# Performance work log

Hardware: AMD Instinct MI355X
Metric: run time of the kernel (lower is better)

Reference implementation:

```python
import jax, jax.numpy as jnp
import numpy as np

EPS = 1e-12
IMU_NOISE_DIAG = np.array([1e-07, 1e-07, 0.01, 0.001], dtype=np.float32)
INIT_COVAR_SQRT = np.array([0, 0, 0, 0, 0, 0, 0.01, 0.01, 0.01, 1e-4, 1e-4, 1e-4,
                            1e-08, 1e-08, 1e-08, 0.1, 0.1, 0.1], dtype=np.float32)
TRANS_SCALE = 5.4
TS2 = TRANS_SCALE * TRANS_SCALE
VIS_INIT_GUESS = 10.0 / TS2
VIS_BETA, VIS_GAMMA = 3.0, 1.0
IMU_BETA, IMU_GAMMA = 4.0, 1.0


def skew3(v):  # (..., 3) -> (..., 3, 3)
    x, y, z = v[..., 0], v[..., 1], v[..., 2]
    o = jnp.zeros_like(x)
    return jnp.stack([jnp.stack([o, -z, y], -1),
                      jnp.stack([z, o, -x], -1),
                      jnp.stack([-y, x, o], -1)], -2)


def exp_SO3(phi):  # (..., 3) -> (..., 3, 3) Rodrigues
    theta2 = jnp.sum(phi * phi, axis=-1)
    theta = jnp.sqrt(theta2)
    small = theta < 1e-8
    th = jnp.where(small, 1.0, theta)
    A = jnp.where(small, 1.0 - theta2 / 6.0, jnp.sin(th) / th)[..., None, None]
    B = jnp.where(small, 0.5 - theta2 / 24.0, (1.0 - jnp.cos(th)) / (th * th))[..., None, None]
    K = skew3(phi)
    return jnp.eye(3, dtype=phi.dtype) + A * K + B * (K @ K)


def force_symmetrical(M):
    Mu = jnp.triu(M)
    n = M.shape[-1]
    return Mu + jnp.swapaxes(Mu, -1, -2) * (1.0 - jnp.eye(n, dtype=M.dtype))


def proc_vis_covar(vis_std):
    # vis_covar_scale is all ones (par.vis_covar_scale = 1.0)
    scale = jnp.ones((6,), dtype=vis_std.dtype)
    diag = VIS_INIT_GUESS * (10.0 ** (VIS_BETA * jnp.tanh(VIS_GAMMA * vis_std)))
    diag = diag / scale[None, :]
    return jax.vmap(jnp.diag)(diag)  # (2B, 6, 6)


def get_imu_noise_covar(imu_noise_weight):
    # Linear(1,4,bias=False) applied to ones(1): just the weight column
    covar = 10.0 ** (IMU_BETA * jnp.tanh(IMU_GAMMA * imu_noise_weight[:, 0]))  # (4,)
    diag = jnp.repeat(jnp.asarray(IMU_NOISE_DIAG), 3) * jnp.repeat(covar, 3)   # (12,)
    return jnp.diag(diag)


def propagate(dts, wa_xyzs, R_ckbts, g_k, imu_noise_covar, P0):
    B = dts.shape[0]
    T = dts.shape[1]
    I3 = jnp.eye(3, dtype=dts.dtype)
    I18 = jnp.eye(18, dtype=dts.dtype)

    def step(P, inp):
        dt, gyro, accel, R = inp  # (B,), (B,3), (B,3), (B,3,3)
        Rt = jnp.swapaxes(R, -1, -2)
        w = gyro  # bw_k = 0
        Rg = jnp.einsum('bij,bj->bi', Rt, g_k)
        a = accel - Rg  # ba_k = 0
        F = jnp.zeros((B, 18, 18), dtype=dt.dtype)
        F = F.at[:, 0:3, 0:3].set(-skew3(w))
        F = F.at[:, 0:3, 12:15].set(-I3)
        F = F.at[:, 3:6, 6:9].set(I3)
        F = F.at[:, 6:9, 0:3].set(-jnp.einsum('bij,bjk->bik', R, skew3(Rg + a)))
        F = F.at[:, 6:9, 9:12].set(-I3)
        F = F.at[:, 6:9, 15:18].set(-R)
        G = jnp.zeros((B, 18, 12), dtype=dt.dtype)
        G = G.at[:, 0:3, 0:3].set(-I3)
        G = G.at[:, 6:9, 6:9].set(-R)
        G = G.at[:, 12:15, 3:6].set(I3)
        G = G.at[:, 15:18, 9:12].set(I3)
        dtb = dt[:, None, None]
        Phi = I18 + F * dtb + 0.5 * (F @ F) * (dtb * dtb)
        Phi = Phi.at[:, 0:3, 0:3].set(jnp.swapaxes(exp_SO3(dt[:, None] * w), -1, -2))
        PhiT = jnp.swapaxes(Phi, -1, -2)
        Q = (Phi @ G @ imu_noise_covar @ jnp.swapaxes(G, -1, -2) @ PhiT) * dtb
        P = force_symmetrical(Phi @ P @ PhiT + Q)
        return P, None

    xs = (jnp.swapaxes(dts, 0, 1),                       # (T, B)
          jnp.swapaxes(wa_xyzs[:, :T, :3], 0, 1),        # (T, B, 3)
          jnp.swapaxes(wa_xyzs[:, :T, 3:], 0, 1),        # (T, B, 3)
          jnp.swapaxes(R_ckbts[:, :T], 0, 1))            # (T, B, 3, 3)
    P, _ = jax.lax.scan(step, P0, xs)
    return P


def update(preimu_rot, preimu_trans, P, vis_rot, vis_trans, vis_covar, H0, H1, v_ck, g_ck):
    B = vis_rot.shape[0]
    residual = jnp.concatenate([vis_rot - preimu_rot, vis_trans - preimu_trans], axis=1)  # (B,6)
    I3 = jnp.eye(3, dtype=vis_rot.dtype)
    H = jnp.zeros((B, 6, 18), dtype=vis_rot.dtype)
    H = H.at[:, 0:3, 0:3].set(H0)
    H = H.at[:, 3:6, 0:3].set(H1)
    H = H.at[:, 3:6, 3:6].set(I3)
    Ht = jnp.swapaxes(H, -1, -2)
    S = H @ P @ Ht + vis_covar                 # (B,6,6)
    K = P @ Ht @ jnp.linalg.inv(S)             # (B,18,6)
    est = K @ residual[..., None]              # (B,18,1)
    phi_e, p_e = est[:, 0:3], est[:, 3:6]
    v_e, g_e = est[:, 6:9], est[:, 9:12]
    ekf_phi = preimu_rot + (H0 @ phi_e)[..., 0]
    ekf_t = preimu_trans + (H1 @ phi_e)[..., 0] + p_e[..., 0]
    return ekf_phi, ekf_t, v_ck + v_e[..., 0], g_ck + g_e[..., 0]


def setup_inputs() -> dict:
    key = jax.random.key(0)
    ks = jax.random.split(key, 16)
    B2 = 8192
    d = {
        'dts': jax.random.uniform(ks[0], (B2, 11), jnp.float32) * 0.01,
        'wa_xyzs': jax.random.normal(ks[1], (B2, 12, 6), jnp.float32),
        'R_ckbts': jax.random.normal(ks[2], (B2, 12, 3, 3), jnp.float32),
        'velocities': jax.random.normal(ks[3], (B2, 3), jnp.float32),
        'gravities': jax.random.normal(ks[4], (B2, 3), jnp.float32),
        'H0': jax.random.normal(ks[5], (B2, 3, 3), jnp.float32),
        'H1': jax.random.normal(ks[6], (B2, 3, 3), jnp.float32),
        'preimu_rot': jax.random.normal(ks[7], (B2, 3), jnp.float32),
        'preimu_trans': jax.random.normal(ks[8], (B2, 3), jnp.float32),
        'vis_rot': jax.random.normal(ks[9], (B2, 3), jnp.float32),
        'vis_trans': jax.random.normal(ks[10], (B2, 3), jnp.float32),
        'vis_rot_std': jax.random.uniform(ks[11], (B2, 3), jnp.float32),
        'vis_trans_std': jax.random.uniform(ks[12], (B2, 3), jnp.float32),
        'init_covar_diag_sqrt': jnp.asarray(INIT_COVAR_SQRT),
        'imu_noise_weight': jnp.zeros((4, 1), jnp.float32),  # train_imu_noise_covar=False -> zeroed
    }
    return d


def reference(dts, wa_xyzs, R_ckbts, velocities, gravities, H0, H1,
              preimu_rot, preimu_trans, vis_rot, vis_trans,
              vis_rot_std, vis_trans_std, init_covar_diag_sqrt, imu_noise_weight):
    B2 = dts.shape[0]
    vis_std = jnp.concatenate([vis_rot_std, vis_trans_std], axis=1)
    vis_covar = proc_vis_covar(vis_std)
    vis_trans = vis_trans * TRANS_SCALE
    imu_noise_covar = get_imu_noise_covar(imu_noise_weight)
    P0_diag = init_covar_diag_sqrt * init_covar_diag_sqrt + EPS
    P0 = jnp.broadcast_to(jnp.diag(P0_diag), (B2, 18, 18))
    P = propagate(dts, wa_xyzs, R_ckbts, gravities, imu_noise_covar, P0)
    ekf_phi, ekf_t, ekf_v, ekf_g = update(preimu_rot, preimu_trans, P,
                                          vis_rot, vis_trans, vis_covar,
                                          H0, H1, velocities, gravities)
    return jnp.concatenate([ekf_phi, ekf_t, ekf_v, ekf_g], axis=1)  # (2B, 12)
```

## Files before the change

### kernel.cpp

```cpp
#include <hip/hip_runtime.h>
#include <math.h>

#define TSTEPS 11
#define PPB 7
#define LPP 9
#define IN_STRIDE 228
#define WSTRIDE 228
#define PHT_OFF 0
#define S6_OFF 144
#define Y_OFF 192
#define EST_OFF 200

#define FENCE_RAW() asm volatile("s_waitcnt lgkmcnt(0)" ::: "memory")
#define FENCE_WAR() asm volatile("" ::: "memory")

__device__ __forceinline__ float sel3(int c, float a, float b, float d) {
    float t = (c == 1) ? b : a;
    return (c == 2) ? d : t;
}

__device__ __forceinline__ size_t umin_sz(size_t a, size_t b) { return a < b ? a : b; }

__global__ void __launch_bounds__(64)
ekf_kernel(const float* __restrict__ dts, const float* __restrict__ wa,
           const float* __restrict__ Rc, const float* __restrict__ vel,
           const float* __restrict__ grav, const float* __restrict__ H0g,
           const float* __restrict__ H1g, const float* __restrict__ prot,
           const float* __restrict__ ptrans, const float* __restrict__ vrot,
           const float* __restrict__ vtrans, const float* __restrict__ vrstd,
           const float* __restrict__ vtstd, const float* __restrict__ icds,
           const float* __restrict__ inw, float* __restrict__ out, int B)
{
    __shared__ __align__(16) float gin[PPB * IN_STRIDE];
    __shared__ __align__(16) float lds[PPB * WSTRIDE];
    const int tid = threadIdx.x;
    const int praw = tid / LPP;
    const int r = tid - praw * LPP;
    const int p = (praw < PPB) ? praw : (PPB - 1);
    const int blk0 = blockIdx.x * PPB;
    const int b0 = blk0 + p;
    const bool valid = (praw < PPB) && (b0 < B);
    const int b = (b0 < B) ? b0 : (B - 1);
    float* L = lds + p * WSTRIDE;
    const float* gi = gin + p * IN_STRIDE;

    {
        const size_t dmax = (size_t)B * 11 - 1;
        for (int e = tid; e < PPB * 11; e += 64) {
            const int pp = e / 11, o = e - pp * 11;
            gin[pp * IN_STRIDE + o * 20] = dts[umin_sz((size_t)blk0 * 11 + e, dmax)];
        }
        const size_t wmax = (size_t)B * 72 - 1;
        for (int e = tid; e < PPB * 66; e += 64) {
            const int pp = e / 66, o = e - pp * 66;
            const int t = o / 6, k = o - t * 6;
            gin[pp * IN_STRIDE + t * 20 + 2 + k] =
                wa[umin_sz((size_t)blk0 * 72 + (size_t)pp * 72 + o, wmax)];
        }
        const size_t rmax = (size_t)B * 108 - 1;
        for (int e = tid; e < PPB * 99; e += 64) {
            const int pp = e / 99, o = e - pp * 99;
            const int t = o / 9, k = o - t * 9;
            gin[pp * IN_STRIDE + t * 20 + 8 + k] =
                Rc[umin_sz((size_t)blk0 * 108 + (size_t)pp * 108 + o, rmax)];
        }
    }

    float h0v[9], h1v[9];
#pragma unroll
    for (int i = 0; i < 9; ++i) { h0v[i] = H0g[(size_t)b * 9 + i]; h1v[i] = H1g[(size_t)b * 9 + i]; }
    const int rc6 = (r < 6) ? r : 5;
    const float* hpr = (rc6 < 3) ? (H0g + (size_t)b * 9 + rc6 * 3)
                                 : (H1g + (size_t)b * 9 + (rc6 - 3) * 3);
    const float hr0 = hpr[0], hr1 = hpr[1], hr2 = hpr[2];
    const float sdv = (rc6 < 3) ? vrstd[(size_t)b * 3 + rc6] : vtstd[(size_t)b * 3 + (rc6 - 3)];
    const float rsa = (rc6 < 3) ? vrot[(size_t)b * 3 + rc6] : vtrans[(size_t)b * 3 + (rc6 - 3)];
    const float rsb = (rc6 < 3) ? prot[(size_t)b * 3 + rc6] : ptrans[(size_t)b * 3 + (rc6 - 3)];
    const float velv = vel[(size_t)b * 3 + ((r >= 6) ? (r - 6) : 0)];

    const float qcA = 1e-7f * exp10f(4.f * tanhf(inw[0]));
    const float qcB = 1e-7f * exp10f(4.f * tanhf(inw[1]));
    const float qcC = 1e-2f * exp10f(4.f * tanhf(inw[2]));
    const float qcD = 1e-3f * exp10f(4.f * tanhf(inw[3]));

    const float g0 = grav[(size_t)b*3+0], g1 = grav[(size_t)b*3+1], g2 = grav[(size_t)b*3+2];

    float np[18], ncr[9];
#pragma unroll
    for (int k = 0; k < 18; ++k) np[k] = 0.f;
#pragma unroll
    for (int k = 0; k < 9; ++k) ncr[k] = 0.f;
    float d_br;
    { const float d0 = icds[r];     np[r] = d0*d0 + 1e-12f;
      const float d1 = icds[9 + r]; d_br  = d1*d1 + 1e-12f; }

    const int cls = (r < 3) ? 0 : ((r < 6) ? 1 : 2);
    const int c3 = r - 3 * cls;

    FENCE_RAW();

    float dt = gi[0];
    float w0, w1, w2, ar0, ar1, ar2, Rm[9];
    {
        const float2 qa = *(const float2*)&gi[2];
        const float2 qb = *(const float2*)&gi[4];
        const float2 qc = *(const float2*)&gi[6];
        w0 = qa.x; w1 = qa.y; w2 = qb.x; ar0 = qb.y; ar1 = qc.x; ar2 = qc.y;
        const float4 r0 = *(const float4*)&gi[8];
        const float4 r1 = *(const float4*)&gi[12];
        Rm[0]=r0.x; Rm[1]=r0.y; Rm[2]=r0.z; Rm[3]=r0.w;
        Rm[4]=r1.x; Rm[5]=r1.y; Rm[6]=r1.z; Rm[7]=r1.w;
        Rm[8]=gi[16];
    }

    for (int t = 0; t < TSTEPS; ++t) {
        const int tn = (t + 1 < TSTEPS) ? (t + 1) : t;
        const float dt_n = gi[tn*20];
        const float2 nqa = *(const float2*)&gi[tn*20 + 2];
        const float2 nqb = *(const float2*)&gi[tn*20 + 4];
        const float2 nqc = *(const float2*)&gi[tn*20 + 6];
        const float4 nr0 = *(const float4*)&gi[tn*20 + 8];
        const float4 nr1 = *(const float4*)&gi[tn*20 + 12];
        const float nr8 = gi[tn*20 + 16];

        const float hdt2 = 0.5f * dt * dt;
        const float Rg0 = Rm[0]*g0 + Rm[3]*g1 + Rm[6]*g2;
        const float Rg1 = Rm[1]*g0 + Rm[4]*g1 + Rm[7]*g2;
        const float Rg2 = Rm[2]*g0 + Rm[5]*g1 + Rm[8]*g2;
        const float a0 = Rg0 + (ar0 - Rg0);
        const float a1 = Rg1 + (ar1 - Rg1);
        const float a2 = Rg2 + (ar2 - Rg2);

        const float p0 = dt*w0, p1 = dt*w1, p2 = dt*w2;
        const float th2 = p0*p0 + p1*p1 + p2*p2;
        const float th4 = th2 * th2;
        const float A  = 1.f - th2*(1.f/6.f)  + th4*(1.f/120.f);
        const float Bc = 0.5f - th2*(1.f/24.f) + th4*(1.f/720.f);
        float E[9];
        E[0] =  Bc*(p0*p0 - th2);  E[1] =  A*p2 + Bc*p0*p1;  E[2] = -A*p1 + Bc*p0*p2;
        E[3] = -A*p2 + Bc*p1*p0;   E[4] =  Bc*(p1*p1 - th2); E[5] =  A*p0 + Bc*p1*p2;
        E[6] =  A*p1 + Bc*p2*p0;   E[7] = -A*p0 + Bc*p2*p1;  E[8] =  Bc*(p2*p2 - th2);
        float N[9];
        N[0] = -(Rm[1]*a2 - Rm[2]*a1);  N[1] = -(Rm[2]*a0 - Rm[0]*a2);  N[2] = -(Rm[0]*a1 - Rm[1]*a0);
        N[3] = -(Rm[4]*a2 - Rm[5]*a1);  N[4] = -(Rm[5]*a0 - Rm[3]*a2);  N[5] = -(Rm[3]*a1 - Rm[4]*a0);
        N[6] = -(Rm[7]*a2 - Rm[8]*a1);  N[7] = -(Rm[8]*a0 - Rm[6]*a2);  N[8] = -(Rm[6]*a1 - Rm[7]*a0);
        float M2[9];
#pragma unroll
        for (int c = 0; c < 3; ++c) {
            const float n0 = N[c*3], n1 = N[c*3+1], n2 = N[c*3+2];
            M2[c*3+0] = dt*n0 - hdt2*(n1*w2 - n2*w1);
            M2[c*3+1] = dt*n1 - hdt2*(n2*w0 - n0*w2);
            M2[c*3+2] = dt*n2 - hdt2*(n0*w1 - n1*w0);
        }

        auto Smv = [&](const float v[18], float o[9]) {
            const float ev0 = E[0]*v[0] + E[1]*v[1] + E[2]*v[2];
            const float ev1 = E[3]*v[0] + E[4]*v[1] + E[5]*v[2];
            const float ev2 = E[6]*v[0] + E[7]*v[1] + E[8]*v[2];
            const float cx0 = w1*v[14] - w2*v[13];
            const float cx1 = w2*v[12] - w0*v[14];
            const float cx2 = w0*v[13] - w1*v[12];
            o[0] = ev0 - dt*v[12] + hdt2*cx0;
            o[1] = ev1 - dt*v[13] + hdt2*cx1;
            o[2] = ev2 - dt*v[14] + hdt2*cx2;
            const float nv0 = N[0]*v[0] + N[1]*v[1] + N[2]*v[2];
            const float nv1 = N[3]*v[0] + N[4]*v[1] + N[5]*v[2];
            const float nv2 = N[6]*v[0] + N[7]*v[1] + N[8]*v[2];
            const float rv0 = Rm[0]*v[15] + Rm[1]*v[16] + Rm[2]*v[17];
            const float rv1 = Rm[3]*v[15] + Rm[4]*v[16] + Rm[5]*v[17];
            const float rv2 = Rm[6]*v[15] + Rm[7]*v[16] + Rm[8]*v[17];
            o[3] = hdt2*nv0 + dt*v[6] - hdt2*v[9]  - hdt2*rv0;
            o[4] = hdt2*nv1 + dt*v[7] - hdt2*v[10] - hdt2*rv1;
            o[5] = hdt2*nv2 + dt*v[8] - hdt2*v[11] - hdt2*rv2;
            const float mv0 = M2[0]*v[0] + M2[1]*v[1] + M2[2]*v[2];
            const float mv1 = M2[3]*v[0] + M2[4]*v[1] + M2[5]*v[2];
            const float mv2 = M2[6]*v[0] + M2[7]*v[1] + M2[8]*v[2];
            const float nw0 = N[0]*v[12] + N[1]*v[13] + N[2]*v[14];
            const float nw1 = N[3]*v[12] + N[4]*v[13] + N[5]*v[14];
            const float nw2 = N[6]*v[12] + N[7]*v[13] + N[8]*v[14];
            o[6] = mv0 - dt*v[9]  - hdt2*nw0 - dt*rv0;
            o[7] = mv1 - dt*v[10] - hdt2*nw1 - dt*rv1;
            o[8] = mv2 - dt*v[11] - hdt2*nw2 - dt*rv2;
        };

        float uca[9];
        Smv(np, uca);

        float ucb[9];
        {
            const float colR0 = sel3(c3, Rm[0], Rm[1], Rm[2]);
            const float colR1 = sel3(c3, Rm[3], Rm[4], Rm[5]);
            const float colR2 = sel3(c3, Rm[6], Rm[7], Rm[8]);
            const float colN0 = sel3(c3, N[0], N[1], N[2]);
            const float colN1 = sel3(c3, N[3], N[4], N[5]);
            const float colN2 = sel3(c3, N[6], N[7], N[8]);
            const float colK0 = sel3(c3, 0.f, -w2,  w1);
            const float colK1 = sel3(c3,  w2, 0.f, -w0);
            const float colK2 = sel3(c3, -w1,  w0, 0.f);
            const float e0c = (c3 == 0) ? 1.f : 0.f;
            const float e1c = (c3 == 1) ? 1.f : 0.f;
            const float e2c = (c3 == 2) ? 1.f : 0.f;
            const float dbdt = d_br * dt, dbh = d_br * hdt2;

            const float s00 = (cls == 1) ? (-dbdt*e0c + dbh*colK0) : 0.f;
            const float s01 = (cls == 1) ? (-dbdt*e1c + dbh*colK1) : 0.f;
            const float s02 = (cls == 1) ? (-dbdt*e2c + dbh*colK2) : 0.f;
            const float s30 = (cls == 0) ? -dbh*e0c : ((cls == 2) ? -dbh*colR0 : 0.f);
            const float s31 = (cls == 0) ? -dbh*e1c : ((cls == 2) ? -dbh*colR1 : 0.f);
            const float s32 = (cls == 0) ? -dbh*e2c : ((cls == 2) ? -dbh*colR2 : 0.f);
            const float s60 = (cls == 0) ? -dbdt*e0c : ((cls == 1) ? -dbh*colN0 : -dbdt*colR0);
            const float s61 = (cls == 0) ? -dbdt*e1c : ((cls == 1) ? -dbh*colN1 : -dbdt*colR1);
            const float s62 = (cls == 0) ? -dbdt*e2c : ((cls == 1) ? -dbh*colN2 : -dbdt*colR2);

            ucb[0] = E[0]*ncr[0] + E[1]*ncr[1] + E[2]*ncr[2] + s00;
            ucb[1] = E[3]*ncr[0] + E[4]*ncr[1] + E[5]*ncr[2] + s01;
            ucb[2] = E[6]*ncr[0] + E[7]*ncr[1] + E[8]*ncr[2] + s02;
            ucb[3] = hdt2*(N[0]*ncr[0] + N[1]*ncr[1] + N[2]*ncr[2]) + dt*ncr[6] + s30;
            ucb[4] = hdt2*(N[3]*ncr[0] + N[4]*ncr[1] + N[5]*ncr[2]) + dt*ncr[7] + s31;
            ucb[5] = hdt2*(N[6]*ncr[0] + N[7]*ncr[1] + N[8]*ncr[2]) + dt*ncr[8] + s32;
            ucb[6] = M2[0]*ncr[0] + M2[1]*ncr[1] + M2[2]*ncr[2] + s60;
            ucb[7] = M2[3]*ncr[0] + M2[4]*ncr[1] + M2[5]*ncr[2] + s61;
            ucb[8] = M2[6]*ncr[0] + M2[7]*ncr[1] + M2[8]*ncr[2] + s62;
        }

#pragma unroll
        for (int i = 0; i < 9; ++i) {
            L[i*20 + r]     = uca[i];
            L[i*20 + 9 + r] = ucb[i];
        }
        FENCE_RAW();

        float ur[18];
        {
            const float4* up = (const float4*)&L[r*20];
            const float4 q0 = up[0], q1 = up[1], q2 = up[2], q3 = up[3];
            const float2 q4 = *(const float2*)&L[r*20 + 16];
            ur[0]=q0.x; ur[1]=q0.y; ur[2]=q0.z; ur[3]=q0.w;
            ur[4]=q1.x; ur[5]=q1.y; ur[6]=q1.z; ur[7]=q1.w;
            ur[8]=q2.x; ur[9]=q2.y; ur[10]=q2.z; ur[11]=q2.w;
            ur[12]=q3.x; ur[13]=q3.y; ur[14]=q3.z; ur[15]=q3.w;
            ur[16]=q4.x; ur[17]=q4.y;
        }

        const float rc0 = sel3(c3, Rm[0], Rm[3], Rm[6]);
        const float rc1 = sel3(c3, Rm[1], Rm[4], Rm[7]);
        const float rc2 = sel3(c3, Rm[2], Rm[5], Rm[8]);
        const float dq = dt * qcC;
        const float q0v = dq * (Rm[0]*rc0 + Rm[1]*rc1 + Rm[2]*rc2);
        const float q1v = dq * (Rm[3]*rc0 + Rm[4]*rc1 + Rm[5]*rc2);
        const float q2v = dq * (Rm[6]*rc0 + Rm[7]*rc1 + Rm[8]*rc2);

        float w9[9];
        Smv(ur, w9);

#pragma unroll
        for (int i = 0; i < 9; ++i)
            np[i] = np[i] + uca[i] + ur[i] + w9[i];
        if (r < 3) np[r] += dt * qcA;
        if (r >= 6) { np[6] += q0v; np[7] += q1v; np[8] += q2v; }
#pragma unroll
        for (int i = 9; i < 18; ++i) np[i] += ur[i];

#pragma unroll
        for (int i = 0; i < 9; ++i) ncr[i] += ucb[i];
        if (r >= 3) d_br += dt * ((r < 6) ? qcB : qcD);

        FENCE_WAR();

        dt = dt_n;
        w0 = nqa.x; w1 = nqa.y; w2 = nqb.x; ar0 = nqb.y; ar1 = nqc.x; ar2 = nqc.y;
        Rm[0]=nr0.x; Rm[1]=nr0.y; Rm[2]=nr0.z; Rm[3]=nr0.w;
        Rm[4]=nr1.x; Rm[5]=nr1.y; Rm[6]=nr1.z; Rm[7]=nr1.w;
        Rm[8]=nr8;
    }

    float phtA[6], phtB[6];
#pragma unroll
    for (int m = 0; m < 3; ++m) {
        phtA[m] = np[0]*h0v[m*3] + np[1]*h0v[m*3+1] + np[2]*h0v[m*3+2];
        phtB[m] = ncr[0]*h0v[m*3] + ncr[1]*h0v[m*3+1] + ncr[2]*h0v[m*3+2];
    }
#pragma unroll
    for (int m = 3; m < 6; ++m) {
        phtA[m] = np[0]*h1v[(m-3)*3] + np[1]*h1v[(m-3)*3+1] + np[2]*h1v[(m-3)*3+2] + np[m];
        phtB[m] = ncr[0]*h1v[(m-3)*3] + ncr[1]*h1v[(m-3)*3+1] + ncr[2]*h1v[(m-3)*3+2] + ncr[m];
    }
#pragma unroll
    for (int m = 0; m < 6; ++m) {
        L[PHT_OFF + r*8 + m]       = phtA[m];
        L[PHT_OFF + (9 + r)*8 + m] = phtB[m];
    }
    FENCE_RAW();

    if (valid && r < 6) {
        const float VIG = (float)(10.0 / (5.4 * 5.4));
#pragma unroll
        for (int n = 0; n < 6; ++n) {
            float v = hr0 * L[PHT_OFF + 0*8 + n] + hr1 * L[PHT_OFF + 1*8 + n]
                    + hr2 * L[PHT_OFF + 2*8 + n];
            if (r >= 3) v += phtA[n];
            if (n == r) v += VIG * exp10f(3.f * tanhf(sdv));
            L[S6_OFF + r*8 + n] = v;
        }
        L[S6_OFF + r*8 + 6] = (r < 3) ? (rsa - rsb) : (rsa * 5.4f - rsb);
    }
    FENCE_RAW();

    if (valid && r == 0) {
        float a[6][7];
        const float* Sb = &L[S6_OFF];
#pragma unroll
        for (int m = 0; m < 6; ++m) {
            const float4 q0 = *(const float4*)&Sb[m*8];
            const float4 q1 = *(const float4*)&Sb[m*8 + 4];
            a[m][0]=q0.x; a[m][1]=q0.y; a[m][2]=q0.z; a[m][3]=q0.w;
            a[m][4]=q1.x; a[m][5]=q1.y; a[m][6]=q1.z;
        }
#pragma unroll
        for (int k = 0; k < 6; ++k) {
#pragma unroll
            for (int j = k + 1; j < 6; ++j) {
                const bool c = fabsf(a[j][k]) > fabsf(a[k][k]);
#pragma unroll
                for (int cc = k; cc < 7; ++cc) {
                    const float hi = c ? a[j][cc] : a[k][cc];
                    const float lo = c ? a[k][cc] : a[j][cc];
                    a[k][cc] = hi; a[j][cc] = lo;
                }
            }
            const float inv = 1.f / a[k][k];
#pragma unroll
            for (int j = 0; j < 6; ++j) {
                if (j == k) continue;
                const float f = a[j][k] * inv;
#pragma unroll
                for (int cc = k + 1; cc < 7; ++cc) a[j][cc] -= f * a[k][cc];
            }
        }
#pragma unroll
        for (int m = 0; m < 6; ++m) L[Y_OFF + m] = a[m][6] / a[m][m];
    }
    FENCE_RAW();

    float ym[6];
#pragma unroll
    for (int m = 0; m < 6; ++m) ym[m] = L[Y_OFF + m];
    float estr = 0.f, est9 = 0.f;
#pragma unroll
    for (int m = 0; m < 6; ++m) { estr += phtA[m]*ym[m]; est9 += phtB[m]*ym[m]; }
    if (valid) {
        L[EST_OFF + r] = estr;
        if (r < 3) L[EST_OFF + 9 + r] = est9;
    }
    FENCE_RAW();

    const float e0 = L[EST_OFF + 0], e1 = L[EST_OFF + 1], e2 = L[EST_OFF + 2];
    if (valid) {
        float o;
        if (r < 3) {
            o = rsb + hr0*e0 + hr1*e1 + hr2*e2;
        } else if (r < 6) {
            o = rsb + hr0*e0 + hr1*e1 + hr2*e2 + estr;
        } else {
            o = velv + estr;
        }
        out[(size_t)b*12 + r] = o;
        if (r < 3) out[(size_t)b*12 + 9 + r] = ((r==0)?g0:((r==1)?g1:g2)) + est9;
    }
}

extern "C" void kernel_launch(void* const* d_in, const int* in_sizes, int n_in,
                              void* d_out, int out_size, void* d_ws, size_t ws_size,
                              hipStream_t stream) {
    const float* dts    = (const float*)d_in[0];
    const float* wa     = (const float*)d_in[1];
    const float* Rc     = (const float*)d_in[2];
    const float* vel    = (const float*)d_in[3];
    const float* grav   = (const float*)d_in[4];
    const float* H0g    = (const float*)d_in[5];
    const float* H1g    = (const float*)d_in[6];
    const float* prot   = (const float*)d_in[7];
    const float* ptrans = (const float*)d_in[8];
    const float* vrot   = (const float*)d_in[9];
    const float* vtrans = (const float*)d_in[10];
    const float* vrstd  = (const float*)d_in[11];
    const float* vtstd  = (const float*)d_in[12];
    const float* icds   = (const float*)d_in[13];
    const float* inw    = (const float*)d_in[14];
    float* outp = (float*)d_out;

    const int B = in_sizes[0] / TSTEPS;
    const int grid = (B + PPB - 1) / PPB;
    hipLaunchKernelGGL(ekf_kernel, dim3(grid), dim3(64), 0, stream,
                       dts, wa, Rc, vel, grav, H0g, H1g, prot, ptrans,
                       vrot, vtrans, vrstd, vtstd, icds, inw, outp, B);
}
```

Measured before the change: 34.50 us.

## Process two EKF problems per lane group to interleave independent work

Each 9-lane group now carries two independent batch elements (A and B), doubling problems per 64-thread block from 7 to 14 and interleaving their propagation and update phases. The aim is to hide the latency of dependent arithmetic and LDS round-trips behind a second independent instruction stream, and to halve the block count. The cost is roughly doubled register pressure and LDS use per block, which can lower occupancy, and fewer blocks for small batches. The two Gauss-Jordan solves run on separate lanes (r==0 and r==1) in parallel.

```diff
diff --git a/kernel.cpp b/kernel.cpp
--- a/kernel.cpp
+++ b/kernel.cpp
@@ -2,7 +2,8 @@
 #include <math.h>
 
 #define TSTEPS 11
-#define PPB 7
+#define GPW 7
+#define PPB 14
 #define LPP 9
 #define IN_STRIDE 228
 #define WSTRIDE 228
@@ -18,8 +19,15 @@
     float t = (c == 1) ? b : a;
     return (c == 2) ? d : t;
 }
-
 __device__ __forceinline__ size_t umin_sz(size_t a, size_t b) { return a < b ? a : b; }
+
+struct SP {
+    float dt, hdt2, w0, w1, w2;
+    float Rm[9], E[9], N[9], M2[9];
+};
+struct UP {
+    float h0v[9], h1v[9], hr0, hr1, hr2, sdv, rsa, rsb, velv;
+};
 
 __global__ void __launch_bounds__(64)
 ekf_kernel(const float* __restrict__ dts, const float* __restrict__ wa,
@@ -36,19 +44,23 @@
     const int tid = threadIdx.x;
     const int praw = tid / LPP;
     const int r = tid - praw * LPP;
-    const int p = (praw < PPB) ? praw : (PPB - 1);
+    const int g = (praw < GPW) ? praw : (GPW - 1);
     const int blk0 = blockIdx.x * PPB;
-    const int b0 = blk0 + p;
-    const bool valid = (praw < PPB) && (b0 < B);
-    const int b = (b0 < B) ? b0 : (B - 1);
-    float* L = lds + p * WSTRIDE;
-    const float* gi = gin + p * IN_STRIDE;
+    const int bA0 = blk0 + g, bB0 = blk0 + GPW + g;
+    const bool validA = (praw < GPW) && (bA0 < B);
+    const bool validB = (praw < GPW) && (bB0 < B);
+    const int bA = (bA0 < B) ? bA0 : (B - 1);
+    const int bB = (bB0 < B) ? bB0 : (B - 1);
+    float* LA = lds + g * WSTRIDE;
+    float* LB = lds + (GPW + g) * WSTRIDE;
+    const float* giA = gin + g * IN_STRIDE;
+    const float* giB = gin + (GPW + g) * IN_STRIDE;
 
     {
         const size_t dmax = (size_t)B * 11 - 1;
         for (int e = tid; e < PPB * 11; e += 64) {
             const int pp = e / 11, o = e - pp * 11;
-            gin[pp * IN_STRIDE + o * 20] = dts[umin_sz((size_t)blk0 * 11 + e, dmax)];
+            gin[pp * IN_STRIDE + o * 20] = dts[umin_sz((size_t)blk0 * 11 + (size_t)pp * 11 + o, dmax)];
         }
         const size_t wmax = (size_t)B * 72 - 1;
         for (int e = tid; e < PPB * 66; e += 64) {
@@ -66,170 +78,133 @@
         }
     }
 
-    float h0v[9], h1v[9];
-#pragma unroll
-    for (int i = 0; i < 9; ++i) { h0v[i] = H0g[(size_t)b * 9 + i]; h1v[i] = H1g[(size_t)b * 9 + i]; }
-    const int rc6 = (r < 6) ? r : 5;
-    const float* hpr = (rc6 < 3) ? (H0g + (size_t)b * 9 + rc6 * 3)
-                                 : (H1g + (size_t)b * 9 + (rc6 - 3) * 3);
-    const float hr0 = hpr[0], hr1 = hpr[1], hr2 = hpr[2];
-    const float sdv = (rc6 < 3) ? vrstd[(size_t)b * 3 + rc6] : vtstd[(size_t)b * 3 + (rc6 - 3)];
-    const float rsa = (rc6 < 3) ? vrot[(size_t)b * 3 + rc6] : vtrans[(size_t)b * 3 + (rc6 - 3)];
-    const float rsb = (rc6 < 3) ? prot[(size_t)b * 3 + rc6] : ptrans[(size_t)b * 3 + (rc6 - 3)];
-    const float velv = vel[(size_t)b * 3 + ((r >= 6) ? (r - 6) : 0)];
-
     const float qcA = 1e-7f * exp10f(4.f * tanhf(inw[0]));
     const float qcB = 1e-7f * exp10f(4.f * tanhf(inw[1]));
     const float qcC = 1e-2f * exp10f(4.f * tanhf(inw[2]));
     const float qcD = 1e-3f * exp10f(4.f * tanhf(inw[3]));
 
-    const float g0 = grav[(size_t)b*3+0], g1 = grav[(size_t)b*3+1], g2 = grav[(size_t)b*3+2];
-
-    float np[18], ncr[9];
-#pragma unroll
-    for (int k = 0; k < 18; ++k) np[k] = 0.f;
-#pragma unroll
-    for (int k = 0; k < 9; ++k) ncr[k] = 0.f;
-    float d_br;
-    { const float d0 = icds[r];     np[r] = d0*d0 + 1e-12f;
-      const float d1 = icds[9 + r]; d_br  = d1*d1 + 1e-12f; }
+    const float gA0 = grav[(size_t)bA*3+0], gA1 = grav[(size_t)bA*3+1], gA2 = grav[(size_t)bA*3+2];
+    const float gB0 = grav[(size_t)bB*3+0], gB1 = grav[(size_t)bB*3+1], gB2 = grav[(size_t)bB*3+2];
+
+    float npA[18], ncrA[9], d_brA, npB[18], ncrB[9], d_brB;
+#pragma unroll
+    for (int k = 0; k < 18; ++k) { npA[k] = 0.f; npB[k] = 0.f; }
+#pragma unroll
+    for (int k = 0; k < 9; ++k) { ncrA[k] = 0.f; ncrB[k] = 0.f; }
+    { const float d0 = icds[r];     npA[r] = d0*d0 + 1e-12f; npB[r] = npA[r];
+      const float d1 = icds[9 + r]; d_brA  = d1*d1 + 1e-12f; d_brB = d_brA; }
 
     const int cls = (r < 3) ? 0 : ((r < 6) ? 1 : 2);
     const int c3 = r - 3 * cls;
 
     FENCE_RAW();
 
-    float dt = gi[0];
-    float w0, w1, w2, ar0, ar1, ar2, Rm[9];
-    {
-        const float2 qa = *(const float2*)&gi[2];
-        const float2 qb = *(const float2*)&gi[4];
-        const float2 qc = *(const float2*)&gi[6];
-        w0 = qa.x; w1 = qa.y; w2 = qb.x; ar0 = qb.y; ar1 = qc.x; ar2 = qc.y;
-        const float4 r0 = *(const float4*)&gi[8];
-        const float4 r1 = *(const float4*)&gi[12];
-        Rm[0]=r0.x; Rm[1]=r0.y; Rm[2]=r0.z; Rm[3]=r0.w;
-        Rm[4]=r1.x; Rm[5]=r1.y; Rm[6]=r1.z; Rm[7]=r1.w;
-        Rm[8]=gi[16];
-    }
-
-    for (int t = 0; t < TSTEPS; ++t) {
-        const int tn = (t + 1 < TSTEPS) ? (t + 1) : t;
-        const float dt_n = gi[tn*20];
-        const float2 nqa = *(const float2*)&gi[tn*20 + 2];
-        const float2 nqb = *(const float2*)&gi[tn*20 + 4];
-        const float2 nqc = *(const float2*)&gi[tn*20 + 6];
-        const float4 nr0 = *(const float4*)&gi[tn*20 + 8];
-        const float4 nr1 = *(const float4*)&gi[tn*20 + 12];
-        const float nr8 = gi[tn*20 + 16];
-
-        const float hdt2 = 0.5f * dt * dt;
-        const float Rg0 = Rm[0]*g0 + Rm[3]*g1 + Rm[6]*g2;
-        const float Rg1 = Rm[1]*g0 + Rm[4]*g1 + Rm[7]*g2;
-        const float Rg2 = Rm[2]*g0 + Rm[5]*g1 + Rm[8]*g2;
+    auto load_sp = [&](const float* gi, int t, float q0, float q1, float q2, SP& s) {
+        const int o = t * 20;
+        s.dt = gi[o];
+        const float2 qa = *(const float2*)&gi[o + 2];
+        const float2 qb = *(const float2*)&gi[o + 4];
+        const float2 qc = *(const float2*)&gi[o + 6];
+        s.w0 = qa.x; s.w1 = qa.y; s.w2 = qb.x;
+        const float ar0 = qb.y, ar1 = qc.x, ar2 = qc.y;
+        const float4 r0 = *(const float4*)&gi[o + 8];
+        const float4 r1 = *(const float4*)&gi[o + 12];
+        s.Rm[0]=r0.x; s.Rm[1]=r0.y; s.Rm[2]=r0.z; s.Rm[3]=r0.w;
+        s.Rm[4]=r1.x; s.Rm[5]=r1.y; s.Rm[6]=r1.z; s.Rm[7]=r1.w;
+        s.Rm[8]=gi[o + 16];
+        s.hdt2 = 0.5f * s.dt * s.dt;
+        const float Rg0 = s.Rm[0]*q0 + s.Rm[3]*q1 + s.Rm[6]*q2;
+        const float Rg1 = s.Rm[1]*q0 + s.Rm[4]*q1 + s.Rm[7]*q2;
+        const float Rg2 = s.Rm[2]*q0 + s.Rm[5]*q1 + s.Rm[8]*q2;
         const float a0 = Rg0 + (ar0 - Rg0);
         const float a1 = Rg1 + (ar1 - Rg1);
         const float a2 = Rg2 + (ar2 - Rg2);
-
-        const float p0 = dt*w0, p1 = dt*w1, p2 = dt*w2;
+        const float p0 = s.dt*s.w0, p1 = s.dt*s.w1, p2 = s.dt*s.w2;
         const float th2 = p0*p0 + p1*p1 + p2*p2;
         const float th4 = th2 * th2;
         const float A  = 1.f - th2*(1.f/6.f)  + th4*(1.f/120.f);
         const float Bc = 0.5f - th2*(1.f/24.f) + th4*(1.f/720.f);
-        float E[9];
-        E[0] =  Bc*(p0*p0 - th2);  E[1] =  A*p2 + Bc*p0*p1;  E[2] = -A*p1 + Bc*p0*p2;
-        E[3] = -A*p2 + Bc*p1*p0;   E[4] =  Bc*(p1*p1 - th2); E[5] =  A*p0 + Bc*p1*p2;
-        E[6] =  A*p1 + Bc*p2*p0;   E[7] = -A*p0 + Bc*p2*p1;  E[8] =  Bc*(p2*p2 - th2);
-        float N[9];
-        N[0] = -(Rm[1]*a2 - Rm[2]*a1);  N[1] = -(Rm[2]*a0 - Rm[0]*a2);  N[2] = -(Rm[0]*a1 - Rm[1]*a0);
-        N[3] = -(Rm[4]*a2 - Rm[5]*a1);  N[4] = -(Rm[5]*a0 - Rm[3]*a2);  N[5] = -(Rm[3]*a1 - Rm[4]*a0);
-        N[6] = -(Rm[7]*a2 - Rm[8]*a1);  N[7] = -(Rm[8]*a0 - Rm[6]*a2);  N[8] = -(Rm[6]*a1 - Rm[7]*a0);
-        float M2[9];
+        s.E[0] =  Bc*(p0*p0 - th2);  s.E[1] =  A*p2 + Bc*p0*p1;  s.E[2] = -A*p1 + Bc*p0*p2;
+        s.E[3] = -A*p2 + Bc*p1*p0;   s.E[4] =  Bc*(p1*p1 - th2); s.E[5] =  A*p0 + Bc*p1*p2;
+        s.E[6] =  A*p1 + Bc*p2*p0;   s.E[7] = -A*p0 + Bc*p2*p1;  s.E[8] =  Bc*(p2*p2 - th2);
+        s.N[0] = -(s.Rm[1]*a2 - s.Rm[2]*a1); s.N[1] = -(s.Rm[2]*a0 - s.Rm[0]*a2); s.N[2] = -(s.Rm[0]*a1 - s.Rm[1]*a0);
+        s.N[3] = -(s.Rm[4]*a2 - s.Rm[5]*a1); s.N[4] = -(s.Rm[5]*a0 - s.Rm[3]*a2); s.N[5] = -(s.Rm[3]*a1 - s.Rm[4]*a0);
+        s.N[6] = -(s.Rm[7]*a2 - s.Rm[8]*a1); s.N[7] = -(s.Rm[8]*a0 - s.Rm[6]*a2); s.N[8] = -(s.Rm[6]*a1 - s.Rm[7]*a0);
 #pragma unroll
         for (int c = 0; c < 3; ++c) {
-            const float n0 = N[c*3], n1 = N[c*3+1], n2 = N[c*3+2];
-            M2[c*3+0] = dt*n0 - hdt2*(n1*w2 - n2*w1);
-            M2[c*3+1] = dt*n1 - hdt2*(n2*w0 - n0*w2);
-            M2[c*3+2] = dt*n2 - hdt2*(n0*w1 - n1*w0);
-        }
-
-        auto Smv = [&](const float v[18], float o[9]) {
-            const float ev0 = E[0]*v[0] + E[1]*v[1] + E[2]*v[2];
-            const float ev1 = E[3]*v[0] + E[4]*v[1] + E[5]*v[2];
-            const float ev2 = E[6]*v[0] + E[7]*v[1] + E[8]*v[2];
-            const float cx0 = w1*v[14] - w2*v[13];
-            const float cx1 = w2*v[12] - w0*v[14];
-            const float cx2 = w0*v[13] - w1*v[12];
-            o[0] = ev0 - dt*v[12] + hdt2*cx0;
-            o[1] = ev1 - dt*v[13] + hdt2*cx1;
-            o[2] = ev2 - dt*v[14] + hdt2*cx2;
-            const float nv0 = N[0]*v[0] + N[1]*v[1] + N[2]*v[2];
-            const float nv1 = N[3]*v[0] + N[4]*v[1] + N[5]*v[2];
-            const float nv2 = N[6]*v[0] + N[7]*v[1] + N[8]*v[2];
-            const float rv0 = Rm[0]*v[15] + Rm[1]*v[16] + Rm[2]*v[17];
-            const float rv1 = Rm[3]*v[15] + Rm[4]*v[16] + Rm[5]*v[17];
-            const float rv2 = Rm[6]*v[15] + Rm[7]*v[16] + Rm[8]*v[17];
-            o[3] = hdt2*nv0 + dt*v[6] - hdt2*v[9]  - hdt2*rv0;
-            o[4] = hdt2*nv1 + dt*v[7] - hdt2*v[10] - hdt2*rv1;
-            o[5] = hdt2*nv2 + dt*v[8] - hdt2*v[11] - hdt2*rv2;
-            const float mv0 = M2[0]*v[0] + M2[1]*v[1] + M2[2]*v[2];
-            const float mv1 = M2[3]*v[0] + M2[4]*v[1] + M2[5]*v[2];
-            const float mv2 = M2[6]*v[0] + M2[7]*v[1] + M2[8]*v[2];
-            const float nw0 = N[0]*v[12] + N[1]*v[13] + N[2]*v[14];
-            const float nw1 = N[3]*v[12] + N[4]*v[13] + N[5]*v[14];
-            const float nw2 = N[6]*v[12] + N[7]*v[13] + N[8]*v[14];
-            o[6] = mv0 - dt*v[9]  - hdt2*nw0 - dt*rv0;
-            o[7] = mv1 - dt*v[10] - hdt2*nw1 - dt*rv1;
-            o[8] = mv2 - dt*v[11] - hdt2*nw2 - dt*rv2;
-        };
-
-        float uca[9];
-        Smv(np, uca);
-
-        float ucb[9];
-        {
-            const float colR0 = sel3(c3, Rm[0], Rm[1], Rm[2]);
-            const float colR1 = sel3(c3, Rm[3], Rm[4], Rm[5]);
-            const float colR2 = sel3(c3, Rm[6], Rm[7], Rm[8]);
-            const float colN0 = sel3(c3, N[0], N[1], N[2]);
-            const float colN1 = sel3(c3, N[3], N[4], N[5]);
-            const float colN2 = sel3(c3, N[6], N[7], N[8]);
-            const float colK0 = sel3(c3, 0.f, -w2,  w1);
-            const float colK1 = sel3(c3,  w2, 0.f, -w0);
-            const float colK2 = sel3(c3, -w1,  w0, 0.f);
-            const float e0c = (c3 == 0) ? 1.f : 0.f;
-            const float e1c = (c3 == 1) ? 1.f : 0.f;
-            const float e2c = (c3 == 2) ? 1.f : 0.f;
-            const float dbdt = d_br * dt, dbh = d_br * hdt2;
-
-            const float s00 = (cls == 1) ? (-dbdt*e0c + dbh*colK0) : 0.f;
-            const float s01 = (cls == 1) ? (-dbdt*e1c + dbh*colK1) : 0.f;
-            const float s02 = (cls == 1) ? (-dbdt*e2c + dbh*colK2) : 0.f;
-            const float s30 = (cls == 0) ? -dbh*e0c : ((cls == 2) ? -dbh*colR0 : 0.f);
-            const float s31 = (cls == 0) ? -dbh*e1c : ((cls == 2) ? -dbh*colR1 : 0.f);
-            const float s32 = (cls == 0) ? -dbh*e2c : ((cls == 2) ? -dbh*colR2 : 0.f);
-            const float s60 = (cls == 0) ? -dbdt*e0c : ((cls == 1) ? -dbh*colN0 : -dbdt*colR0);
-            const float s61 = (cls == 0) ? -dbdt*e1c : ((cls == 1) ? -dbh*colN1 : -dbdt*colR1);
-            const float s62 = (cls == 0) ? -dbdt*e2c : ((cls == 1) ? -dbh*colN2 : -dbdt*colR2);
-
-            ucb[0] = E[0]*ncr[0] + E[1]*ncr[1] + E[2]*ncr[2] + s00;
-            ucb[1] = E[3]*ncr[0] + E[4]*ncr[1] + E[5]*ncr[2] + s01;
-            ucb[2] = E[6]*ncr[0] + E[7]*ncr[1] + E[8]*ncr[2] + s02;
-            ucb[3] = hdt2*(N[0]*ncr[0] + N[1]*ncr[1] + N[2]*ncr[2]) + dt*ncr[6] + s30;
-            ucb[4] = hdt2*(N[3]*ncr[0] + N[4]*ncr[1] + N[5]*ncr[2]) + dt*ncr[7] + s31;
-            ucb[5] = hdt2*(N[6]*ncr[0] + N[7]*ncr[1] + N[8]*ncr[2]) + dt*ncr[8] + s32;
-            ucb[6] = M2[0]*ncr[0] + M2[1]*ncr[1] + M2[2]*ncr[2] + s60;
-            ucb[7] = M2[3]*ncr[0] + M2[4]*ncr[1] + M2[5]*ncr[2] + s61;
-            ucb[8] = M2[6]*ncr[0] + M2[7]*ncr[1] + M2[8]*ncr[2] + s62;
-        }
-
-#pragma unroll
-        for (int i = 0; i < 9; ++i) {
-            L[i*20 + r]     = uca[i];
-            L[i*20 + 9 + r] = ucb[i];
-        }
-        FENCE_RAW();
-
+            const float n0 = s.N[c*3], n1 = s.N[c*3+1], n2 = s.N[c*3+2];
+            s.M2[c*3+0] = s.dt*n0 - s.hdt2*(n1*s.w2 - n2*s.w1);
+            s.M2[c*3+1] = s.dt*n1 - s.hdt2*(n2*s.w0 - n0*s.w2);
+            s.M2[c*3+2] = s.dt*n2 - s.hdt2*(n0*s.w1 - n1*s.w0);
+        }
+    };
+
+    auto Smv = [&](const SP& s, const float v[18], float o[9]) {
+        const float ev0 = s.E[0]*v[0] + s.E[1]*v[1] + s.E[2]*v[2];
+        const float ev1 = s.E[3]*v[0] + s.E[4]*v[1] + s.E[5]*v[2];
+        const float ev2 = s.E[6]*v[0] + s.E[7]*v[1] + s.E[8]*v[2];
+        const float cx0 = s.w1*v[14] - s.w2*v[13];
+        const float cx1 = s.w2*v[12] - s.w0*v[14];
+        const float cx2 = s.w0*v[13] - s.w1*v[12];
+        o[0] = ev0 - s.dt*v[12] + s.hdt2*cx0;
+        o[1] = ev1 - s.dt*v[13] + s.hdt2*cx1;
+        o[2] = ev2 - s.dt*v[14] + s.hdt2*cx2;
+        const float nv0 = s.N[0]*v[0] + s.N[1]*v[1] + s.N[2]*v[2];
+        const float nv1 = s.N[3]*v[0] + s.N[4]*v[1] + s.N[5]*v[2];
+        const float nv2 = s.N[6]*v[0] + s.N[7]*v[1] + s.N[8]*v[2];
+        const float rv0 = s.Rm[0]*v[15] + s.Rm[1]*v[16] + s.Rm[2]*v[17];
+        const float rv1 = s.Rm[3]*v[15] + s.Rm[4]*v[16] + s.Rm[5]*v[17];
+        const float rv2 = s.Rm[6]*v[15] + s.Rm[7]*v[16] + s.Rm[8]*v[17];
+        o[3] = s.hdt2*nv0 + s.dt*v[6] - s.hdt2*v[9]  - s.hdt2*rv0;
+        o[4] = s.hdt2*nv1 + s.dt*v[7] - s.hdt2*v[10] - s.hdt2*rv1;
+        o[5] = s.hdt2*nv2 + s.dt*v[8] - s.hdt2*v[11] - s.hdt2*rv2;
+        const float mv0 = s.M2[0]*v[0] + s.M2[1]*v[1] + s.M2[2]*v[2];
+        const float mv1 = s.M2[3]*v[0] + s.M2[4]*v[1] + s.M2[5]*v[2];
+        const float mv2 = s.M2[6]*v[0] + s.M2[7]*v[1] + s.M2[8]*v[2];
+        const float nw0 = s.N[0]*v[12] + s.N[1]*v[13] + s.N[2]*v[14];
+        const float nw1 = s.N[3]*v[12] + s.N[4]*v[13] + s.N[5]*v[14];
+        const float nw2 = s.N[6]*v[12] + s.N[7]*v[13] + s.N[8]*v[14];
+        o[6] = mv0 - s.dt*v[9]  - s.hdt2*nw0 - s.dt*rv0;
+        o[7] = mv1 - s.dt*v[10] - s.hdt2*nw1 - s.dt*rv1;
+        o[8] = mv2 - s.dt*v[11] - s.hdt2*nw2 - s.dt*rv2;
+    };
+
+    auto ucb_col = [&](const SP& s, const float ncr[9], float d_br, float ucb[9]) {
+        const float colR0 = sel3(c3, s.Rm[0], s.Rm[1], s.Rm[2]);
+        const float colR1 = sel3(c3, s.Rm[3], s.Rm[4], s.Rm[5]);
+        const float colR2 = sel3(c3, s.Rm[6], s.Rm[7], s.Rm[8]);
+        const float colN0 = sel3(c3, s.N[0], s.N[1], s.N[2]);
+        const float colN1 = sel3(c3, s.N[3], s.N[4], s.N[5]);
+        const float colN2 = sel3(c3, s.N[6], s.N[7], s.N[8]);
+        const float colK0 = sel3(c3, 0.f, -s.w2,  s.w1);
+        const float colK1 = sel3(c3,  s.w2, 0.f, -s.w0);
+        const float colK2 = sel3(c3, -s.w1,  s.w0, 0.f);
+        const float e0c = (c3 == 0) ? 1.f : 0.f;
+        const float e1c = (c3 == 1) ? 1.f : 0.f;
+        const float e2c = (c3 == 2) ? 1.f : 0.f;
+        const float dbdt = d_br * s.dt, dbh = d_br * s.hdt2;
+        const float s00 = (cls == 1) ? (-dbdt*e0c + dbh*colK0) : 0.f;
+        const float s01 = (cls == 1) ? (-dbdt*e1c + dbh*colK1) : 0.f;
+        const float s02 = (cls == 1) ? (-dbdt*e2c + dbh*colK2) : 0.f;
+        const float s30 = (cls == 0) ? -dbh*e0c : ((cls == 2) ? -dbh*colR0 : 0.f);
+        const float s31 = (cls == 0) ? -dbh*e1c : ((cls == 2) ? -dbh*colR1 : 0.f);
+        const float s32 = (cls == 0) ? -dbh*e2c : ((cls == 2) ? -dbh*colR2 : 0.f);
+        const float s60 = (cls == 0) ? -dbdt*e0c : ((cls == 1) ? -dbh*colN0 : -dbdt*colR0);
+        const float s61 = (cls == 0) ? -dbdt*e1c : ((cls == 1) ? -dbh*colN1 : -dbdt*colR1);
+        const float s62 = (cls == 0) ? -dbdt*e2c : ((cls == 1) ? -dbh*colN2 : -dbdt*colR2);
+        ucb[0] = s.E[0]*ncr[0] + s.E[1]*ncr[1] + s.E[2]*ncr[2] + s00;
+        ucb[1] = s.E[3]*ncr[0] + s.E[4]*ncr[1] + s.E[5]*ncr[2] + s01;
+        ucb[2] = s.E[6]*ncr[0] + s.E[7]*ncr[1] + s.E[8]*ncr[2] + s02;
+        ucb[3] = s.hdt2*(s.N[0]*ncr[0] + s.N[1]*ncr[1] + s.N[2]*ncr[2]) + s.dt*ncr[6] + s30;
+        ucb[4] = s.hdt2*(s.N[3]*ncr[0] + s.N[4]*ncr[1] + s.N[5]*ncr[2]) + s.dt*ncr[7] + s31;
+        ucb[5] = s.hdt2*(s.N[6]*ncr[0] + s.N[7]*ncr[1] + s.N[8]*ncr[2]) + s.dt*ncr[8] + s32;
+        ucb[6] = s.M2[0]*ncr[0] + s.M2[1]*ncr[1] + s.M2[2]*ncr[2] + s60;
+        ucb[7] = s.M2[3]*ncr[0] + s.M2[4]*ncr[1] + s.M2[5]*ncr[2] + s61;
+        ucb[8] = s.M2[6]*ncr[0] + s.M2[7]*ncr[1] + s.M2[8]*ncr[2] + s62;
+    };
+
+    auto phaseB = [&](const SP& s, float* L, const float uca[9], const float ucb[9],
+                      float np[18], float ncr[9], float& d_br) {
         float ur[18];
         {
             const float4* up = (const float4*)&L[r*20];
@@ -241,131 +216,179 @@
             ur[12]=q3.x; ur[13]=q3.y; ur[14]=q3.z; ur[15]=q3.w;
             ur[16]=q4.x; ur[17]=q4.y;
         }
-
-        const float rc0 = sel3(c3, Rm[0], Rm[3], Rm[6]);
-        const float rc1 = sel3(c3, Rm[1], Rm[4], Rm[7]);
-        const float rc2 = sel3(c3, Rm[2], Rm[5], Rm[8]);
-        const float dq = dt * qcC;
-        const float q0v = dq * (Rm[0]*rc0 + Rm[1]*rc1 + Rm[2]*rc2);
-        const float q1v = dq * (Rm[3]*rc0 + Rm[4]*rc1 + Rm[5]*rc2);
-        const float q2v = dq * (Rm[6]*rc0 + Rm[7]*rc1 + Rm[8]*rc2);
-
+        const float rc0 = sel3(c3, s.Rm[0], s.Rm[3], s.Rm[6]);
+        const float rc1 = sel3(c3, s.Rm[1], s.Rm[4], s.Rm[7]);
+        const float rc2 = sel3(c3, s.Rm[2], s.Rm[5], s.Rm[8]);
+        const float dq = s.dt * qcC;
+        const float q0v = dq * (s.Rm[0]*rc0 + s.Rm[1]*rc1 + s.Rm[2]*rc2);
+        const float q1v = dq * (s.Rm[3]*rc0 + s.Rm[4]*rc1 + s.Rm[5]*rc2);
+        const float q2v = dq * (s.Rm[6]*rc0 + s.Rm[7]*rc1 + s.Rm[8]*rc2);
         float w9[9];
-        Smv(ur, w9);
-
-#pragma unroll
-        for (int i = 0; i < 9; ++i)
-            np[i] = np[i] + uca[i] + ur[i] + w9[i];
-        if (r < 3) np[r] += dt * qcA;
+        Smv(s, ur, w9);
+#pragma unroll
+        for (int i = 0; i < 9; ++i) np[i] = np[i] + uca[i] + ur[i] + w9[i];
+        if (r < 3) np[r] += s.dt * qcA;
         if (r >= 6) { np[6] += q0v; np[7] += q1v; np[8] += q2v; }
 #pragma unroll
         for (int i = 9; i < 18; ++i) np[i] += ur[i];
-
 #pragma unroll
         for (int i = 0; i < 9; ++i) ncr[i] += ucb[i];
-        if (r >= 3) d_br += dt * ((r < 6) ? qcB : qcD);
-
+        if (r >= 3) d_br += s.dt * ((r < 6) ? qcB : qcD);
+    };
+
+    for (int t = 0; t < TSTEPS; ++t) {
+        SP sA, sB;
+        load_sp(giA, t, gA0, gA1, gA2, sA);
+        load_sp(giB, t, gB0, gB1, gB2, sB);
+        float ucaA[9], ucbA[9], ucaB[9], ucbB[9];
+        Smv(sA, npA, ucaA);
+        ucb_col(sA, ncrA, d_brA, ucbA);
+        Smv(sB, npB, ucaB);
+        ucb_col(sB, ncrB, d_brB, ucbB);
+#pragma unroll
+        for (int i = 0; i < 9; ++i) {
+            LA[i*20 + r]     = ucaA[i];
+            LA[i*20 + 9 + r] = ucbA[i];
+            LB[i*20 + r]     = ucaB[i];
+            LB[i*20 + 9 + r] = ucbB[i];
+        }
+        FENCE_RAW();
+        phaseB(sA, LA, ucaA, ucbA, npA, ncrA, d_brA);
+        phaseB(sB, LB, ucaB, ucbB, npB, ncrB, d_brB);
         FENCE_WAR();
-
-        dt = dt_n;
-        w0 = nqa.x; w1 = nqa.y; w2 = nqb.x; ar0 = nqb.y; ar1 = nqc.x; ar2 = nqc.y;
-        Rm[0]=nr0.x; Rm[1]=nr0.y; Rm[2]=nr0.z; Rm[3]=nr0.w;
-        Rm[4]=nr1.x; Rm[5]=nr1.y; Rm[6]=nr1.z; Rm[7]=nr1.w;
-        Rm[8]=nr8;
-    }
-
-    float phtA[6], phtB[6];
-#pragma unroll
-    for (int m = 0; m < 3; ++m) {
-        phtA[m] = np[0]*h0v[m*3] + np[1]*h0v[m*3+1] + np[2]*h0v[m*3+2];
-        phtB[m] = ncr[0]*h0v[m*3] + ncr[1]*h0v[m*3+1] + ncr[2]*h0v[m*3+2];
-    }
-#pragma unroll
-    for (int m = 3; m < 6; ++m) {
-        phtA[m] = np[0]*h1v[(m-3)*3] + np[1]*h1v[(m-3)*3+1] + np[2]*h1v[(m-3)*3+2] + np[m];
-        phtB[m] = ncr[0]*h1v[(m-3)*3] + ncr[1]*h1v[(m-3)*3+1] + ncr[2]*h1v[(m-3)*3+2] + ncr[m];
-    }
-#pragma unroll
-    for (int m = 0; m < 6; ++m) {
-        L[PHT_OFF + r*8 + m]       = phtA[m];
-        L[PHT_OFF + (9 + r)*8 + m] = phtB[m];
-    }
+    }
+
+    auto load_up = [&](int b, UP& u) {
+#pragma unroll
+        for (int i = 0; i < 9; ++i) { u.h0v[i] = H0g[(size_t)b*9 + i]; u.h1v[i] = H1g[(size_t)b*9 + i]; }
+        const int rc6 = (r < 6) ? r : 5;
+        const float* hpr = (rc6 < 3) ? (H0g + (size_t)b*9 + rc6*3)
+                                     : (H1g + (size_t)b*9 + (rc6-3)*3);
+        u.hr0 = hpr[0]; u.hr1 = hpr[1]; u.hr2 = hpr[2];
+        u.sdv = (rc6 < 3) ? vrstd[(size_t)b*3 + rc6] : vtstd[(size_t)b*3 + (rc6-3)];
+        u.rsa = (rc6 < 3) ? vrot[(size_t)b*3 + rc6] : vtrans[(size_t)b*3 + (rc6-3)];
+        u.rsb = (rc6 < 3) ? prot[(size_t)b*3 + rc6] : ptrans[(size_t)b*3 + (rc6-3)];
+        u.velv = vel[(size_t)b*3 + ((r >= 6) ? (r-6) : 0)];
+    };
+    UP uA, uB;
+    load_up(bA, uA);
+    load_up(bB, uB);
+
+    float phtRA[6], phtSA[6], phtRB[6], phtSB[6];
+    auto pht = [&](const UP& u, const float np[18], const float ncr[9], float* L,
+                   float phtR[6], float phtS[6]) {
+#pragma unroll
+        for (int m = 0; m < 3; ++m) {
+            phtR[m] = np[0]*u.h0v[m*3] + np[1]*u.h0v[m*3+1] + np[2]*u.h0v[m*3+2];
+            phtS[m] = ncr[0]*u.h0v[m*3] + ncr[1]*u.h0v[m*3+1] + ncr[2]*u.h0v[m*3+2];
+        }
+#pragma unroll
+        for (int m = 3; m < 6; ++m) {
+            phtR[m] = np[0]*u.h1v[(m-3)*3] + np[1]*u.h1v[(m-3)*3+1] + np[2]*u.h1v[(m-3)*3+2] + np[m];
+            phtS[m] = ncr[0]*u.h1v[(m-3)*3] + ncr[1]*u.h1v[(m-3)*3+1] + ncr[2]*u.h1v[(m-3)*3+2] + ncr[m];
+        }
+#pragma unroll
+        for (int m = 0; m < 6; ++m) {
+            L[PHT_OFF + r*8 + m]       = phtR[m];
+            L[PHT_OFF + (9 + r)*8 + m] = phtS[m];
+        }
+    };
+    pht(uA, npA, ncrA, LA, phtRA, phtSA);
+    pht(uB, npB, ncrB, LB, phtRB, phtSB);
     FENCE_RAW();
 
-    if (valid && r < 6) {
-        const float VIG = (float)(10.0 / (5.4 * 5.4));
-#pragma unroll
-        for (int n = 0; n < 6; ++n) {
-            float v = hr0 * L[PHT_OFF + 0*8 + n] + hr1 * L[PHT_OFF + 1*8 + n]
-                    + hr2 * L[PHT_OFF + 2*8 + n];
-            if (r >= 3) v += phtA[n];
-            if (n == r) v += VIG * exp10f(3.f * tanhf(sdv));
-            L[S6_OFF + r*8 + n] = v;
-        }
-        L[S6_OFF + r*8 + 6] = (r < 3) ? (rsa - rsb) : (rsa * 5.4f - rsb);
-    }
+    auto s6build = [&](const UP& u, bool valid, const float phtR[6], float* L) {
+        if (valid && r < 6) {
+            const float VIG = (float)(10.0 / (5.4 * 5.4));
+#pragma unroll
+            for (int n = 0; n < 6; ++n) {
+                float v = u.hr0 * L[PHT_OFF + 0*8 + n] + u.hr1 * L[PHT_OFF + 1*8 + n]
+                        + u.hr2 * L[PHT_OFF + 2*8 + n];
+                if (r >= 3) v += phtR[n];
+                if (n == r) v += VIG * exp10f(3.f * tanhf(u.sdv));
+                L[S6_OFF + r*8 + n] = v;
+            }
+            L[S6_OFF + r*8 + 6] = (r < 3) ? (u.rsa - u.rsb) : (u.rsa * 5.4f - u.rsb);
+        }
+    };
+    s6build(uA, validA, phtRA, LA);
+    s6build(uB, validB, phtRB, LB);
     FENCE_RAW();
 
-    if (valid && r == 0) {
-        float a[6][7];
-        const float* Sb = &L[S6_OFF];
-#pragma unroll
-        for (int m = 0; m < 6; ++m) {
-            const float4 q0 = *(const float4*)&Sb[m*8];
-            const float4 q1 = *(const float4*)&Sb[m*8 + 4];
-            a[m][0]=q0.x; a[m][1]=q0.y; a[m][2]=q0.z; a[m][3]=q0.w;
-            a[m][4]=q1.x; a[m][5]=q1.y; a[m][6]=q1.z;
-        }
-#pragma unroll
-        for (int k = 0; k < 6; ++k) {
-#pragma unroll
-            for (int j = k + 1; j < 6; ++j) {
-                const bool c = fabsf(a[j][k]) > fabsf(a[k][k]);
-#pragma unroll
-                for (int cc = k; cc < 7; ++cc) {
-                    const float hi = c ? a[j][cc] : a[k][cc];
-                    const float lo = c ? a[k][cc] : a[j][cc];
-                    a[k][cc] = hi; a[j][cc] = lo;
+    {
+        const bool doSolve = (praw < GPW) && ((r == 0) ? validA : ((r == 1) ? validB : false));
+        if (doSolve) {
+            float* Sb = (r == 0) ? &LA[S6_OFF] : &LB[S6_OFF];
+            float* Yp = (r == 0) ? &LA[Y_OFF] : &LB[Y_OFF];
+            float a[6][7];
+#pragma unroll
+            for (int m = 0; m < 6; ++m) {
+                const float4 q0 = *(const float4*)&Sb[m*8];
+                const float4 q1 = *(const float4*)&Sb[m*8 + 4];
+                a[m][0]=q0.x; a[m][1]=q0.y; a[m][2]=q0.z; a[m][3]=q0.w;
+                a[m][4]=q1.x; a[m][5]=q1.y; a[m][6]=q1.z;
+            }
+#pragma unroll
+            for (int k = 0; k < 6; ++k) {
+#pragma unroll
+                for (int j = k + 1; j < 6; ++j) {
+                    const bool c = fabsf(a[j][k]) > fabsf(a[k][k]);
+#pragma unroll
+                    for (int cc = k; cc < 7; ++cc) {
+                        const float hi = c ? a[j][cc] : a[k][cc];
+                        const float lo = c ? a[k][cc] : a[j][cc];
+                        a[k][cc] = hi; a[j][cc] = lo;
+                    }
+                }
+                const float inv = 1.f / a[k][k];
+#pragma unroll
+                for (int j = 0; j < 6; ++j) {
+                    if (j == k) continue;
+                    const float f = a[j][k] * inv;
+#pragma unroll
+                    for (int cc = k + 1; cc < 7; ++cc) a[j][cc] -= f * a[k][cc];
                 }
             }
-            const float inv = 1.f / a[k][k];
-#pragma unroll
-            for (int j = 0; j < 6; ++j) {
-                if (j == k) continue;
-                const float f = a[j][k] * inv;
-#pragma unroll
-                for (int cc = k + 1; cc < 7; ++cc) a[j][cc] -= f * a[k][cc];
-            }
-        }
-#pragma unroll
-        for (int m = 0; m < 6; ++m) L[Y_OFF + m] = a[m][6] / a[m][m];
+#pragma unroll
+            for (int m = 0; m < 6; ++m) Yp[m] = a[m][6] / a[m][m];
+        }
     }
     FENCE_RAW();
 
-    float ym[6];
-#pragma unroll
-    for (int m = 0; m < 6; ++m) ym[m] = L[Y_OFF + m];
-    float estr = 0.f, est9 = 0.f;
-#pragma unroll
-    for (int m = 0; m < 6; ++m) { estr += phtA[m]*ym[m]; est9 += phtB[m]*ym[m]; }
-    if (valid) {
-        L[EST_OFF + r] = estr;
-        if (r < 3) L[EST_OFF + 9 + r] = est9;
-    }
+    float ymA[6], ymB[6];
+#pragma unroll
+    for (int m = 0; m < 6; ++m) { ymA[m] = LA[Y_OFF + m]; ymB[m] = LB[Y_OFF + m]; }
+    float estrA = 0.f, est9A = 0.f, estrB = 0.f, est9B = 0.f;
+#pragma unroll
+    for (int m = 0; m < 6; ++m) {
+        estrA += phtRA[m]*ymA[m]; est9A += phtSA[m]*ymA[m];
+        estrB += phtRB[m]*ymB[m]; est9B += phtSB[m]*ymB[m];
+    }
+    if (validA) LA[EST_OFF + r] = estrA;
+    if (validB) LB[EST_OFF + r] = estrB;
     FENCE_RAW();
 
-    const float e0 = L[EST_OFF + 0], e1 = L[EST_OFF + 1], e2 = L[EST_OFF + 2];
-    if (valid) {
-        float o;
-        if (r < 3) {
-            o = rsb + hr0*e0 + hr1*e1 + hr2*e2;
-        } else if (r < 6) {
-            o = rsb + hr0*e0 + hr1*e1 + hr2*e2 + estr;
-        } else {
-            o = velv + estr;
-        }
-        out[(size_t)b*12 + r] = o;
-        if (r < 3) out[(size_t)b*12 + 9 + r] = ((r==0)?g0:((r==1)?g1:g2)) + est9;
+    {
+        const float e0 = LA[EST_OFF + 0], e1 = LA[EST_OFF + 1], e2 = LA[EST_OFF + 2];
+        if (validA) {
+            float o;
+            if (r < 3)      o = uA.rsb + uA.hr0*e0 + uA.hr1*e1 + uA.hr2*e2;
+            else if (r < 6) o = uA.rsb + uA.hr0*e0 + uA.hr1*e1 + uA.hr2*e2 + estrA;
+            else            o = uA.velv + estrA;
+            out[(size_t)bA*12 + r] = o;
+            if (r < 3) out[(size_t)bA*12 + 9 + r] = ((r==0)?gA0:((r==1)?gA1:gA2)) + est9A;
+        }
+    }
+    {
+        const float e0 = LB[EST_OFF + 0], e1 = LB[EST_OFF + 1], e2 = LB[EST_OFF + 2];
+        if (validB) {
+            float o;
+            if (r < 3)      o = uB.rsb + uB.hr0*e0 + uB.hr1*e1 + uB.hr2*e2;
+            else if (r < 6) o = uB.rsb + uB.hr0*e0 + uB.hr1*e1 + uB.hr2*e2 + estrB;
+            else            o = uB.velv + estrB;
+            out[(size_t)bB*12 + r] = o;
+            if (r < 3) out[(size_t)bB*12 + 9 + r] = ((r==0)?gB0:((r==1)?gB1:gB2)) + est9B;
+        }
     }
 }
 
```

Result: slower. 42.77 us (+24.0%).
